# Kernel tuning notes

Hardware: AMD Instinct MI355X
Metric: run time of the kernel (lower is better)

Reference implementation:

```python
import jax, jax.numpy as jnp
import numpy as np

E = 8        # num_local_experts
H = 2048     # hidden_size
I = 4096     # intermediate_size
TOP_K = 1    # num_experts_per_tok
B, S = 2, 1024


def setup_inputs() -> dict:
    key = jax.random.key(0)
    ks = jax.random.split(key, 8)
    sc = 0.02
    return {
        "hidden_states": jax.random.normal(ks[0], (B, S, H), dtype=jnp.float32),
        "router_w": jax.random.normal(ks[1], (E, H), dtype=jnp.float32) * sc,      # torch Linear weight [out,in]
        "gate_up_proj": jax.random.normal(ks[2], (E, H, 2 * I), dtype=jnp.float32) * sc,
        "down_proj": jax.random.normal(ks[3], (E, I, H), dtype=jnp.float32) * sc,
        "shared_gate": jax.random.normal(ks[4], (H, I), dtype=jnp.float32) * sc,
        "shared_up": jax.random.normal(ks[5], (H, I), dtype=jnp.float32) * sc,
        "shared_down": jax.random.normal(ks[6], (I, H), dtype=jnp.float32) * sc,
    }


def reference(hidden_states, router_w, gate_up_proj, down_proj, shared_gate, shared_up, shared_down):
    x = hidden_states.reshape(-1, H)                      # [T, H]
    T = x.shape[0]

    # Router: top-k logits kept, rest -> -inf, then sigmoid (Llama4 sigmoid routing)
    logits = jnp.einsum('th,eh->te', x, router_w)          # [T, E]
    topv, topi = jax.lax.top_k(logits, TOP_K)
    scores = jnp.full_like(logits, -jnp.inf)
    scores = scores.at[jnp.arange(T)[:, None], topi].set(topv)
    router_scores = jax.nn.sigmoid(scores.astype(jnp.float32)).astype(x.dtype).T  # [E, T]

    # Dense dispatch: every token goes to every expert, scaled by its (mostly-zero) score
    routed_in = x[None, :, :] * router_scores[:, :, None]  # [E, T, H]

    # Per-expert gated MLP as one grouped einsum
    gu = jnp.einsum('eth,ehf->etf', routed_in, gate_up_proj)   # [E, T, 2I]
    gate, up = gu[..., :I], gu[..., I:]
    routed_out = jnp.einsum('eti,eih->eth', jax.nn.silu(gate) * up, down_proj)  # [E, T, H]

    # Shared expert on raw tokens
    shared = (jax.nn.silu(x @ shared_gate) * (x @ shared_up)) @ shared_down     # [T, H]

    # scatter_add over full index range == sum over expert axis
    out = shared + routed_out.sum(axis=0)
    return out, router_scores
```

## Files before the change

kernel.cpp:

```cpp
#include <hip/hip_runtime.h>
#include <hip/hip_bf16.h>

#define NE 8
#define TT 2048
#define HD 2048
#define ID 4096

typedef __attribute__((ext_vector_type(8))) short bf16x8;
typedef __attribute__((ext_vector_type(4))) float f32x4;
typedef __attribute__((ext_vector_type(4))) unsigned int u32x4;
typedef __attribute__((ext_vector_type(4))) unsigned short u16x4;
typedef __attribute__((ext_vector_type(8))) unsigned short u16x8;

__device__ __forceinline__ unsigned short f2bf(float f) {
  unsigned int u = __builtin_bit_cast(unsigned int, f);
  u += 0x7FFFu + ((u >> 16) & 1u);
  return (unsigned short)(u >> 16);
}

__global__ void init_kernel(int* counts) {
  if (threadIdx.x < NE) counts[threadIdx.x] = 0;
}

__global__ __launch_bounds__(256) void router_kernel(
    const float* __restrict__ x, const float* __restrict__ rw,
    float* __restrict__ rs_out, unsigned short* __restrict__ xb,
    unsigned short* __restrict__ xsb, int* __restrict__ counts,
    int* __restrict__ tlist) {
  const int t = blockIdx.x;
  const int tid = threadIdx.x;
  const float* xr = x + (size_t)t * HD;
  float acc[NE];
#pragma unroll
  for (int e = 0; e < NE; ++e) acc[e] = 0.f;
  for (int h = tid; h < HD; h += 256) {
    float xv = xr[h];
#pragma unroll
    for (int e = 0; e < NE; ++e) acc[e] += xv * rw[e * HD + h];
  }
#pragma unroll
  for (int e = 0; e < NE; ++e) {
#pragma unroll
    for (int off = 32; off > 0; off >>= 1) acc[e] += __shfl_down(acc[e], off);
  }
  __shared__ float part[4][NE];
  __shared__ int sE;
  __shared__ float sS;
  const int wave = tid >> 6, lane = tid & 63;
  if (lane == 0) {
#pragma unroll
    for (int e = 0; e < NE; ++e) part[wave][e] = acc[e];
  }
  __syncthreads();
  if (tid == 0) {
    float best = -3.4e38f;
    int be = 0;
#pragma unroll
    for (int e = 0; e < NE; ++e) {
      float v = part[0][e] + part[1][e] + part[2][e] + part[3][e];
      if (v > best) { best = v; be = e; }
    }
    float s = 1.f / (1.f + expf(-best));
    sE = be;
    sS = s;
    int pos = atomicAdd(&counts[be], 1);
    tlist[be * TT + pos] = t;
  }
  __syncthreads();
  if (tid < NE) rs_out[tid * TT + t] = (tid == sE) ? sS : 0.f;
  const float s = sS;
  for (int h = tid; h < HD; h += 256) {
    float f = xr[h];
    xb[(size_t)t * HD + h] = f2bf(f);
    xsb[(size_t)t * HD + h] = f2bf(f * s);
  }
}

__global__ __launch_bounds__(256) void tconv_kernel(
    const float* __restrict__ shg, const float* __restrict__ shu,
    const float* __restrict__ shd, unsigned short* __restrict__ shgT,
    unsigned short* __restrict__ shuT, unsigned short* __restrict__ shdT) {
  const int z = blockIdx.z;
  const float* src;
  unsigned short* dst;
  int K, N;
  if (z == 0)      { src = shg; dst = shgT; K = HD; N = ID; }
  else if (z == 1) { src = shu; dst = shuT; K = HD; N = ID; }
  else             { src = shd; dst = shdT; K = ID; N = HD; }
  const int kb = blockIdx.y * 64, nb = blockIdx.x * 64;
  if (kb >= K || nb >= N) return;
  __shared__ unsigned short tile[64][68];
  const int tid = threadIdx.x;
  const int rr = tid >> 4, cc = (tid & 15) * 4;
#pragma unroll
  for (int it = 0; it < 4; ++it) {
    int r = rr + it * 16;
    f32x4 v = *(const f32x4*)(const void*)(src + (size_t)(kb + r) * N + nb + cc);
    tile[r][cc + 0] = f2bf(v[0]);
    tile[r][cc + 1] = f2bf(v[1]);
    tile[r][cc + 2] = f2bf(v[2]);
    tile[r][cc + 3] = f2bf(v[3]);
  }
  __syncthreads();
  const int nr = tid >> 2, kc = (tid & 3) * 16;
#pragma unroll
  for (int h = 0; h < 2; ++h) {
    u16x8 w;
#pragma unroll
    for (int j = 0; j < 8; ++j) w[j] = tile[kc + h * 8 + j][nr];
    *(u16x8*)(void*)(dst + (size_t)(nb + nr) * K + kb + kc + h * 8) = w;
  }
}

__global__ __launch_bounds__(256) void gateup_kernel(
    const unsigned short* __restrict__ xb, const unsigned short* __restrict__ xsb,
    const float* __restrict__ gup, const float* __restrict__ shg,
    const float* __restrict__ shu, const unsigned short* __restrict__ shgT,
    const unsigned short* __restrict__ shuT, const int* __restrict__ counts,
    const int* __restrict__ tlist, unsigned short* __restrict__ hsh,
    unsigned short* __restrict__ hrt, const int shbf) {
  const int bz = blockIdx.z;
  const bool sh = (bz == NE);
  const int cnt = sh ? TT : counts[bz];
  const int row0 = blockIdx.y * 128;
  if (row0 >= cnt) return;
  const int n0 = blockIdx.x * 64;
  const unsigned short* Aptr = sh ? xb : xsb;
  const bool bfb = sh && (shbf != 0);
  const float *B1, *B2;
  size_t ldb;
  const unsigned short *T1 = nullptr, *T2 = nullptr;
  if (sh) {
    B1 = shg + n0; B2 = shu + n0; ldb = ID;
    T1 = shgT + (size_t)n0 * HD; T2 = shuT + (size_t)n0 * HD;
  } else {
    const float* base = gup + (size_t)bz * HD * 2 * ID;
    B1 = base + n0; B2 = base + ID + n0; ldb = 2 * ID;
  }
  unsigned short* hout = sh ? hsh : hrt;

  __shared__ int toks[128];
  __shared__ __align__(16) unsigned short As[2][128][40];
  __shared__ __align__(16) unsigned short Bg[2][64][40];
  __shared__ __align__(16) unsigned short Bu[2][64][40];

  const int tid = threadIdx.x;
  if (tid < 128) {
    int r = row0 + tid;
    toks[tid] = (r < cnt) ? (sh ? r : tlist[bz * TT + r]) : -1;
  }
  __syncthreads();

  const int lane = tid & 63, wave = tid >> 6;
  const int wm = (wave >> 1) * 64, wn = (wave & 1) * 32;
  const int rA0 = tid >> 2, cA = (tid & 3) * 8, rA1 = rA0 + 64;
  const int tok0 = toks[rA0], tok1 = toks[rA1];
  const unsigned short* ap0 = Aptr + ((tok0 >= 0) ? (size_t)tok0 * HD : 0) + cA;
  const unsigned short* ap1 = Aptr + ((tok1 >= 0) ? (size_t)tok1 * HD : 0) + cA;
  const int nB = tid & 63;
  const int kq0 = tid >> 6;
  const int fm = lane & 15, q = lane >> 4;
  const int nrT = tid >> 2, kcT = (tid & 3) * 8;

  const f32x4 zf = {0.f, 0.f, 0.f, 0.f};
  const u32x4 z4 = {0u, 0u, 0u, 0u};
  f32x4 accg[4][2], accu[4][2];
#pragma unroll
  for (int a = 0; a < 4; ++a)
#pragma unroll
    for (int b = 0; b < 2; ++b) { accg[a][b] = zf; accu[a][b] = zf; }

  u32x4 ra0, ra1, tb1, tb2;
  f32x4 rg0, rg1, ru0, ru1;

#define GU_LOAD(K0)                                                            \
  do {                                                                         \
    ra0 = (tok0 >= 0) ? *(const u32x4*)(const void*)(ap0 + (K0)) : z4;         \
    ra1 = (tok1 >= 0) ? *(const u32x4*)(const void*)(ap1 + (K0)) : z4;         \
    if (bfb) {                                                                 \
      tb1 = *(const u32x4*)(const void*)(T1 + (size_t)nrT * HD + (K0) + kcT);  \
      tb2 = *(const u32x4*)(const void*)(T2 + (size_t)nrT * HD + (K0) + kcT);  \
    } else {                                                                   \
      const float* p1 = B1 + (size_t)((K0) + kq0 * 4) * ldb + nB;              \
      const float* p1b = p1 + 16 * ldb;                                        \
      rg0[0] = p1[0]; rg0[1] = p1[ldb]; rg0[2] = p1[2 * ldb]; rg0[3] = p1[3 * ldb]; \
      rg1[0] = p1b[0]; rg1[1] = p1b[ldb]; rg1[2] = p1b[2 * ldb]; rg1[3] = p1b[3 * ldb]; \
      const float* p2 = B2 + (size_t)((K0) + kq0 * 4) * ldb + nB;              \
      const float* p2b = p2 + 16 * ldb;                                        \
      ru0[0] = p2[0]; ru0[1] = p2[ldb]; ru0[2] = p2[2 * ldb]; ru0[3] = p2[3 * ldb]; \
      ru1[0] = p2b[0]; ru1[1] = p2b[ldb]; ru1[2] = p2b[2 * ldb]; ru1[3] = p2b[3 * ldb]; \
    }                                                                          \
  } while (0)

#define GU_WRITE(BUF)                                                          \
  do {                                                                         \
    *(u32x4*)(void*)&As[BUF][rA0][cA] = ra0;                                   \
    *(u32x4*)(void*)&As[BUF][rA1][cA] = ra1;                                   \
    if (bfb) {                                                                 \
      *(u32x4*)(void*)&Bg[BUF][nrT][kcT] = tb1;                                \
      *(u32x4*)(void*)&Bu[BUF][nrT][kcT] = tb2;                                \
    } else {                                                                   \
      u16x4 w;                                                                 \
      w[0] = f2bf(rg0[0]); w[1] = f2bf(rg0[1]); w[2] = f2bf(rg0[2]); w[3] = f2bf(rg0[3]); \
      *(u16x4*)(void*)&Bg[BUF][nB][kq0 * 4] = w;                               \
      w[0] = f2bf(rg1[0]); w[1] = f2bf(rg1[1]); w[2] = f2bf(rg1[2]); w[3] = f2bf(rg1[3]); \
      *(u16x4*)(void*)&Bg[BUF][nB][kq0 * 4 + 16] = w;                          \
      w[0] = f2bf(ru0[0]); w[1] = f2bf(ru0[1]); w[2] = f2bf(ru0[2]); w[3] = f2bf(ru0[3]); \
      *(u16x4*)(void*)&Bu[BUF][nB][kq0 * 4] = w;                               \
      w[0] = f2bf(ru1[0]); w[1] = f2bf(ru1[1]); w[2] = f2bf(ru1[2]); w[3] = f2bf(ru1[3]); \
      *(u16x4*)(void*)&Bu[BUF][nB][kq0 * 4 + 16] = w;                          \
    }                                                                          \
  } while (0)

  GU_LOAD(0);
  GU_WRITE(0);
  GU_LOAD(32);
  asm volatile("s_waitcnt lgkmcnt(0)" ::: "memory");
  __builtin_amdgcn_sched_barrier(0);
  __builtin_amdgcn_s_barrier();

  for (int t = 0; t < HD / 32; ++t) {
    const int cur = t & 1;
    bf16x8 af[4], bgf[2], buf2[2];
#pragma unroll
    for (int mt = 0; mt < 4; ++mt)
      af[mt] = __builtin_bit_cast(bf16x8,
               *(const u32x4*)(const void*)&As[cur][wm + mt * 16 + fm][q * 8]);
#pragma unroll
    for (int nt = 0; nt < 2; ++nt) {
      bgf[nt] = __builtin_bit_cast(bf16x8,
                *(const u32x4*)(const void*)&Bg[cur][wn + nt * 16 + fm][q * 8]);
      buf2[nt] = __builtin_bit_cast(bf16x8,
                 *(const u32x4*)(const void*)&Bu[cur][wn + nt * 16 + fm][q * 8]);
    }
    if (t + 1 < HD / 32) GU_WRITE(cur ^ 1);
    if (t + 2 < HD / 32) GU_LOAD((t + 2) * 32);
    __builtin_amdgcn_s_setprio(1);
#pragma unroll
    for (int mt = 0; mt < 4; ++mt)
#pragma unroll
      for (int nt = 0; nt < 2; ++nt) {
        accg[mt][nt] = __builtin_amdgcn_mfma_f32_16x16x32_bf16(af[mt], bgf[nt], accg[mt][nt], 0, 0, 0);
        accu[mt][nt] = __builtin_amdgcn_mfma_f32_16x16x32_bf16(af[mt], buf2[nt], accu[mt][nt], 0, 0, 0);
      }
    __builtin_amdgcn_s_setprio(0);
    asm volatile("s_waitcnt lgkmcnt(0)" ::: "memory");
    __builtin_amdgcn_sched_barrier(0);
    __builtin_amdgcn_s_barrier();
  }
#undef GU_LOAD
#undef GU_WRITE

#pragma unroll
  for (int mt = 0; mt < 4; ++mt)
#pragma unroll
    for (int nt = 0; nt < 2; ++nt)
#pragma unroll
      for (int r = 0; r < 4; ++r) {
        int ml = wm + mt * 16 + q * 4 + r;
        if (row0 + ml < cnt) {
          int tok = toks[ml];
          int n = n0 + wn + nt * 16 + fm;
          float g = accg[mt][nt][r], u = accu[mt][nt][r];
          float hv = g / (1.f + __expf(-g)) * u;
          hout[(size_t)tok * ID + n] = f2bf(hv);
        }
      }
}

__global__ __launch_bounds__(256) void down_kernel(
    const unsigned short* __restrict__ Ah, const float* __restrict__ Bbase,
    const unsigned short* __restrict__ BT, const int* __restrict__ counts,
    const int* __restrict__ tlist, float* __restrict__ out,
    const int routed, const int shbf) {
  const int e = blockIdx.z;
  const int cnt = routed ? counts[e] : TT;
  const int row0 = blockIdx.y * 128;
  if (row0 >= cnt) return;
  const int n0 = blockIdx.x * 64;
  const bool bfb = (!routed) && (shbf != 0);
  const float* B = routed ? (Bbase + (size_t)e * ID * HD + n0) : (Bbase + n0);
  const unsigned short* T = BT + (size_t)n0 * ID;

  __shared__ int toks[128];
  __shared__ __align__(16) unsigned short As[2][128][40];
  __shared__ __align__(16) unsigned short Bs[2][64][40];

  const int tid = threadIdx.x;
  if (tid < 128) {
    int r = row0 + tid;
    toks[tid] = (r < cnt) ? (routed ? tlist[e * TT + r] : r) : -1;
  }
  __syncthreads();

  const int lane = tid & 63, wave = tid >> 6;
  const int wm = (wave >> 1) * 64, wn = (wave & 1) * 32;
  const int rA0 = tid >> 2, cA = (tid & 3) * 8, rA1 = rA0 + 64;
  const int tok0 = toks[rA0], tok1 = toks[rA1];
  const unsigned short* ap0 = Ah + ((tok0 >= 0) ? (size_t)tok0 * ID : 0) + cA;
  const unsigned short* ap1 = Ah + ((tok1 >= 0) ? (size_t)tok1 * ID : 0) + cA;
  const int nB = tid & 63;
  const int kq0 = tid >> 6;
  const int fm = lane & 15, q = lane >> 4;
  const int nrT = tid >> 2, kcT = (tid & 3) * 8;

  const f32x4 zf = {0.f, 0.f, 0.f, 0.f};
  const u32x4 z4 = {0u, 0u, 0u, 0u};
  f32x4 acc[4][2];
#pragma unroll
  for (int a = 0; a < 4; ++a)
#pragma unroll
    for (int b = 0; b < 2; ++b) acc[a][b] = zf;

  u32x4 ra0, ra1, tb;
  f32x4 rb0, rb1;

#define DN_LOAD(K0)                                                            \
  do {                                                                         \
    ra0 = (tok0 >= 0) ? *(const u32x4*)(const void*)(ap0 + (K0)) : z4;         \
    ra1 = (tok1 >= 0) ? *(const u32x4*)(const void*)(ap1 + (K0)) : z4;         \
    if (bfb) {                                                                 \
      tb = *(const u32x4*)(const void*)(T + (size_t)nrT * ID + (K0) + kcT);    \
    } else {                                                                   \
      const float* p = B + (size_t)((K0) + kq0 * 4) * HD + nB;                 \
      const float* pb = p + 16 * HD;                                           \
      rb0[0] = p[0]; rb0[1] = p[HD]; rb0[2] = p[2 * HD]; rb0[3] = p[3 * HD];   \
      rb1[0] = pb[0]; rb1[1] = pb[HD]; rb1[2] = pb[2 * HD]; rb1[3] = pb[3 * HD]; \
    }                                                                          \
  } while (0)

#define DN_WRITE(BUF)                                                          \
  do {                                                                         \
    *(u32x4*)(void*)&As[BUF][rA0][cA] = ra0;                                   \
    *(u32x4*)(void*)&As[BUF][rA1][cA] = ra1;                                   \
    if (bfb) {                                                                 \
      *(u32x4*)(void*)&Bs[BUF][nrT][kcT] = tb;                                 \
    } else {                                                                   \
      u16x4 w;                                                                 \
      w[0] = f2bf(rb0[0]); w[1] = f2bf(rb0[1]); w[2] = f2bf(rb0[2]); w[3] = f2bf(rb0[3]); \
      *(u16x4*)(void*)&Bs[BUF][nB][kq0 * 4] = w;                               \
      w[0] = f2bf(rb1[0]); w[1] = f2bf(rb1[1]); w[2] = f2bf(rb1[2]); w[3] = f2bf(rb1[3]); \
      *(u16x4*)(void*)&Bs[BUF][nB][kq0 * 4 + 16] = w;                          \
    }                                                                          \
  } while (0)

  DN_LOAD(0);
  DN_WRITE(0);
  DN_LOAD(32);
  asm volatile("s_waitcnt lgkmcnt(0)" ::: "memory");
  __builtin_amdgcn_sched_barrier(0);
  __builtin_amdgcn_s_barrier();

  for (int t = 0; t < ID / 32; ++t) {
    const int cur = t & 1;
    bf16x8 af[4], bfr[2];
#pragma unroll
    for (int mt = 0; mt < 4; ++mt)
      af[mt] = __builtin_bit_cast(bf16x8,
               *(const u32x4*)(const void*)&As[cur][wm + mt * 16 + fm][q * 8]);
#pragma unroll
    for (int nt = 0; nt < 2; ++nt)
      bfr[nt] = __builtin_bit_cast(bf16x8,
                *(const u32x4*)(const void*)&Bs[cur][wn + nt * 16 + fm][q * 8]);
    if (t + 1 < ID / 32) DN_WRITE(cur ^ 1);
    if (t + 2 < ID / 32) DN_LOAD((t + 2) * 32);
    __builtin_amdgcn_s_setprio(1);
#pragma unroll
    for (int mt = 0; mt < 4; ++mt)
#pragma unroll
      for (int nt = 0; nt < 2; ++nt)
        acc[mt][nt] = __builtin_amdgcn_mfma_f32_16x16x32_bf16(af[mt], bfr[nt], acc[mt][nt], 0, 0, 0);
    __builtin_amdgcn_s_setprio(0);
    asm volatile("s_waitcnt lgkmcnt(0)" ::: "memory");
    __builtin_amdgcn_sched_barrier(0);
    __builtin_amdgcn_s_barrier();
  }
#undef DN_LOAD
#undef DN_WRITE

#pragma unroll
  for (int mt = 0; mt < 4; ++mt)
#pragma unroll
    for (int nt = 0; nt < 2; ++nt)
#pragma unroll
      for (int r = 0; r < 4; ++r) {
        int ml = wm + mt * 16 + q * 4 + r;
        if (row0 + ml < cnt) {
          int tok = toks[ml];
          int n = n0 + wn + nt * 16 + fm;
          float v = acc[mt][nt][r];
          float* o = out + (size_t)tok * HD + n;
          if (routed) *o += v; else *o = v;
        }
      }
}

extern "C" void kernel_launch(void* const* d_in, const int* in_sizes, int n_in,
                              void* d_out, int out_size, void* d_ws, size_t ws_size,
                              hipStream_t stream) {
  const float* x   = (const float*)d_in[0];
  const float* rw  = (const float*)d_in[1];
  const float* gup = (const float*)d_in[2];
  const float* dwn = (const float*)d_in[3];
  const float* shg = (const float*)d_in[4];
  const float* shu = (const float*)d_in[5];
  const float* shd = (const float*)d_in[6];
  float* out = (float*)d_out;

  char* ws = (char*)d_ws;
  int* counts = (int*)ws;
  int* tlist = (int*)(ws + 1024);
  unsigned short* xb  = (unsigned short*)(ws + (1 << 17));
  unsigned short* xsb = (unsigned short*)(ws + (1 << 17) + 8388608);
  unsigned short* hsh = (unsigned short*)(ws + (1 << 17) + 16777216);
  unsigned short* hrt = (unsigned short*)(ws + (1 << 17) + 33554432);
  const size_t WB = (size_t)(1 << 17) + 50331648;
  unsigned short* shgT = (unsigned short*)(ws + WB);
  unsigned short* shuT = (unsigned short*)(ws + WB + 16777216);
  unsigned short* shdT = (unsigned short*)(ws + WB + 33554432);
  const size_t need = WB + 3ull * 16777216ull;
  const int shbf = (ws_size >= need) ? 1 : 0;

  hipLaunchKernelGGL(init_kernel, dim3(1), dim3(64), 0, stream, counts);
  hipLaunchKernelGGL(router_kernel, dim3(TT), dim3(256), 0, stream,
                     x, rw, out + (size_t)TT * HD, xb, xsb, counts, tlist);
  if (shbf)
    hipLaunchKernelGGL(tconv_kernel, dim3(64, 64, 3), dim3(256), 0, stream,
                       shg, shu, shd, shgT, shuT, shdT);
  hipLaunchKernelGGL(gateup_kernel, dim3(ID / 64, TT / 128, NE + 1), dim3(256), 0, stream,
                     xb, xsb, gup, shg, shu, shgT, shuT, counts, tlist, hsh, hrt, shbf);
  hipLaunchKernelGGL(down_kernel, dim3(HD / 64, TT / 128, 1), dim3(256), 0, stream,
                     hsh, shd, shdT, counts, tlist, out, 0, shbf);
  hipLaunchKernelGGL(down_kernel, dim3(HD / 64, TT / 128, NE), dim3(256), 0, stream,
                     hrt, dwn, shdT, counts, tlist, out, 1, shbf);
}
```

Baseline: 1.351 ms.

## Split MoE GEMM kernels into specialized routed/shared variants and reorder pipeline

```diff
diff --git a/kernel.cpp b/kernel.cpp
--- a/kernel.cpp
+++ b/kernel.cpp
@@ -9,13 +9,12 @@
 typedef __attribute__((ext_vector_type(8))) short bf16x8;
 typedef __attribute__((ext_vector_type(4))) float f32x4;
 typedef __attribute__((ext_vector_type(4))) unsigned int u32x4;
+typedef __attribute__((ext_vector_type(2))) unsigned int u32x2;
 typedef __attribute__((ext_vector_type(4))) unsigned short u16x4;
 typedef __attribute__((ext_vector_type(8))) unsigned short u16x8;
 
 __device__ __forceinline__ unsigned short f2bf(float f) {
-  unsigned int u = __builtin_bit_cast(unsigned int, f);
-  u += 0x7FFFu + ((u >> 16) & 1u);
-  return (unsigned short)(u >> 16);
+  return __builtin_bit_cast(unsigned short, __float2bfloat16(f));
 }
 
 __global__ void init_kernel(int* counts) {
@@ -112,42 +111,29 @@
   }
 }
 
-__global__ __launch_bounds__(256) void gateup_kernel(
-    const unsigned short* __restrict__ xb, const unsigned short* __restrict__ xsb,
-    const float* __restrict__ gup, const float* __restrict__ shg,
-    const float* __restrict__ shu, const unsigned short* __restrict__ shgT,
-    const unsigned short* __restrict__ shuT, const int* __restrict__ counts,
-    const int* __restrict__ tlist, unsigned short* __restrict__ hsh,
-    unsigned short* __restrict__ hrt, const int shbf) {
-  const int bz = blockIdx.z;
-  const bool sh = (bz == NE);
-  const int cnt = sh ? TT : counts[bz];
+__global__ __launch_bounds__(256) void gu_routed_kernel(
+    const unsigned short* __restrict__ xsb, const float* __restrict__ gup,
+    const int* __restrict__ counts, const int* __restrict__ tlist,
+    unsigned short* __restrict__ hrt) {
+  const int e = blockIdx.z;
+  const int cnt = counts[e];
   const int row0 = blockIdx.y * 128;
   if (row0 >= cnt) return;
   const int n0 = blockIdx.x * 64;
-  const unsigned short* Aptr = sh ? xb : xsb;
-  const bool bfb = sh && (shbf != 0);
-  const float *B1, *B2;
-  size_t ldb;
-  const unsigned short *T1 = nullptr, *T2 = nullptr;
-  if (sh) {
-    B1 = shg + n0; B2 = shu + n0; ldb = ID;
-    T1 = shgT + (size_t)n0 * HD; T2 = shuT + (size_t)n0 * HD;
-  } else {
-    const float* base = gup + (size_t)bz * HD * 2 * ID;
-    B1 = base + n0; B2 = base + ID + n0; ldb = 2 * ID;
-  }
-  unsigned short* hout = sh ? hsh : hrt;
+  const float* Bb = gup + (size_t)e * HD * (2 * ID);
+  const float* B1 = Bb + n0;
+  const float* B2 = Bb + ID + n0;
+  const size_t ldb = 2 * ID;
 
   __shared__ int toks[128];
   __shared__ __align__(16) unsigned short As[2][128][40];
-  __shared__ __align__(16) unsigned short Bg[2][64][40];
-  __shared__ __align__(16) unsigned short Bu[2][64][40];
+  __shared__ __align__(16) unsigned short Bg[2][64][36];
+  __shared__ __align__(16) unsigned short Bu[2][64][36];
 
   const int tid = threadIdx.x;
   if (tid < 128) {
     int r = row0 + tid;
-    toks[tid] = (r < cnt) ? (sh ? r : tlist[bz * TT + r]) : -1;
+    toks[tid] = (r < cnt) ? tlist[e * TT + r] : -1;
   }
   __syncthreads();
 
@@ -155,15 +141,145 @@
   const int wm = (wave >> 1) * 64, wn = (wave & 1) * 32;
   const int rA0 = tid >> 2, cA = (tid & 3) * 8, rA1 = rA0 + 64;
   const int tok0 = toks[rA0], tok1 = toks[rA1];
-  const unsigned short* ap0 = Aptr + ((tok0 >= 0) ? (size_t)tok0 * HD : 0) + cA;
-  const unsigned short* ap1 = Aptr + ((tok1 >= 0) ? (size_t)tok1 * HD : 0) + cA;
+  const unsigned short* ap0 = xsb + ((tok0 >= 0) ? (size_t)tok0 * HD : 0) + cA;
+  const unsigned short* ap1 = xsb + ((tok1 >= 0) ? (size_t)tok1 * HD : 0) + cA;
+  const int nB = tid & 63;
+  const int kq0 = tid >> 6;
+  const int fm = lane & 15, q = lane >> 4;
+
+  const f32x4 zf = {0.f, 0.f, 0.f, 0.f};
+  const u32x4 z4 = {0u, 0u, 0u, 0u};
+  f32x4 accg[4][2], accu[4][2];
+#pragma unroll
+  for (int a = 0; a < 4; ++a)
+#pragma unroll
+    for (int b = 0; b < 2; ++b) { accg[a][b] = zf; accu[a][b] = zf; }
+
+  u32x4 ra0, ra1;
+  f32x4 rg0, rg1, ru0, ru1;
+
+#define LD(K0)                                                                 \
+  do {                                                                         \
+    ra0 = (tok0 >= 0) ? *(const u32x4*)(const void*)(ap0 + (K0)) : z4;         \
+    ra1 = (tok1 >= 0) ? *(const u32x4*)(const void*)(ap1 + (K0)) : z4;         \
+    const float* p1 = B1 + (size_t)((K0) + kq0 * 4) * ldb + nB;                \
+    const float* p1b = p1 + 16 * ldb;                                          \
+    rg0[0] = p1[0]; rg0[1] = p1[ldb]; rg0[2] = p1[2 * ldb]; rg0[3] = p1[3 * ldb]; \
+    rg1[0] = p1b[0]; rg1[1] = p1b[ldb]; rg1[2] = p1b[2 * ldb]; rg1[3] = p1b[3 * ldb]; \
+    const float* p2 = B2 + (size_t)((K0) + kq0 * 4) * ldb + nB;                \
+    const float* p2b = p2 + 16 * ldb;                                          \
+    ru0[0] = p2[0]; ru0[1] = p2[ldb]; ru0[2] = p2[2 * ldb]; ru0[3] = p2[3 * ldb]; \
+    ru1[0] = p2b[0]; ru1[1] = p2b[ldb]; ru1[2] = p2b[2 * ldb]; ru1[3] = p2b[3 * ldb]; \
+  } while (0)
+
+#define WR(BUF)                                                                \
+  do {                                                                         \
+    *(u32x4*)(void*)&As[BUF][rA0][cA] = ra0;                                   \
+    *(u32x4*)(void*)&As[BUF][rA1][cA] = ra1;                                   \
+    u16x4 w;                                                                   \
+    w[0] = f2bf(rg0[0]); w[1] = f2bf(rg0[1]); w[2] = f2bf(rg0[2]); w[3] = f2bf(rg0[3]); \
+    *(u16x4*)(void*)&Bg[BUF][nB][kq0 * 4] = w;                                 \
+    w[0] = f2bf(rg1[0]); w[1] = f2bf(rg1[1]); w[2] = f2bf(rg1[2]); w[3] = f2bf(rg1[3]); \
+    *(u16x4*)(void*)&Bg[BUF][nB][kq0 * 4 + 16] = w;                            \
+    w[0] = f2bf(ru0[0]); w[1] = f2bf(ru0[1]); w[2] = f2bf(ru0[2]); w[3] = f2bf(ru0[3]); \
+    *(u16x4*)(void*)&Bu[BUF][nB][kq0 * 4] = w;                                 \
+    w[0] = f2bf(ru1[0]); w[1] = f2bf(ru1[1]); w[2] = f2bf(ru1[2]); w[3] = f2bf(ru1[3]); \
+    *(u16x4*)(void*)&Bu[BUF][nB][kq0 * 4 + 16] = w;                            \
+  } while (0)
+
+  LD(0);
+  WR(0);
+  LD(32);
+  asm volatile("s_waitcnt lgkmcnt(0)" ::: "memory");
+  __builtin_amdgcn_sched_barrier(0);
+  __builtin_amdgcn_s_barrier();
+
+  constexpr int NT = HD / 32;
+  for (int t = 0; t < NT; ++t) {
+    const int cur = t & 1;
+    bf16x8 af[4], bgf[2], bud[2];
+#pragma unroll
+    for (int mt = 0; mt < 4; ++mt)
+      af[mt] = __builtin_bit_cast(bf16x8,
+               *(const u32x4*)(const void*)&As[cur][wm + mt * 16 + fm][q * 8]);
+#pragma unroll
+    for (int nt = 0; nt < 2; ++nt) {
+      const unsigned short* bp = &Bg[cur][wn + nt * 16 + fm][q * 8];
+      u32x2 lo = *(const u32x2*)(const void*)bp;
+      u32x2 hi = *(const u32x2*)(const void*)(bp + 4);
+      u32x4 v; v[0] = lo[0]; v[1] = lo[1]; v[2] = hi[0]; v[3] = hi[1];
+      bgf[nt] = __builtin_bit_cast(bf16x8, v);
+      const unsigned short* bp2 = &Bu[cur][wn + nt * 16 + fm][q * 8];
+      lo = *(const u32x2*)(const void*)bp2;
+      hi = *(const u32x2*)(const void*)(bp2 + 4);
+      v[0] = lo[0]; v[1] = lo[1]; v[2] = hi[0]; v[3] = hi[1];
+      bud[nt] = __builtin_bit_cast(bf16x8, v);
+    }
+    __builtin_amdgcn_s_setprio(1);
+#pragma unroll
+    for (int mt = 0; mt < 4; ++mt)
+#pragma unroll
+      for (int nt = 0; nt < 2; ++nt) {
+        accg[mt][nt] = __builtin_amdgcn_mfma_f32_16x16x32_bf16(af[mt], bgf[nt], accg[mt][nt], 0, 0, 0);
+        accu[mt][nt] = __builtin_amdgcn_mfma_f32_16x16x32_bf16(af[mt], bud[nt], accu[mt][nt], 0, 0, 0);
+      }
+    __builtin_amdgcn_s_setprio(0);
+    __builtin_amdgcn_sched_barrier(0);
+    if (t + 1 < NT) WR(cur ^ 1);
+    if (t + 2 < NT) LD((t + 2) * 32);
+    asm volatile("s_waitcnt lgkmcnt(0)" ::: "memory");
+    __builtin_amdgcn_sched_barrier(0);
+    __builtin_amdgcn_s_barrier();
+  }
+#undef LD
+#undef WR
+
+#pragma unroll
+  for (int mt = 0; mt < 4; ++mt)
+#pragma unroll
+    for (int nt = 0; nt < 2; ++nt)
+#pragma unroll
+      for (int r = 0; r < 4; ++r) {
+        int ml = wm + mt * 16 + q * 4 + r;
+        if (row0 + ml < cnt) {
+          int tok = toks[ml];
+          int n = n0 + wn + nt * 16 + fm;
+          float g = accg[mt][nt][r], u = accu[mt][nt][r];
+          float hv = g / (1.f + __expf(-g)) * u;
+          hrt[(size_t)tok * ID + n] = f2bf(hv);
+        }
+      }
+}
+
+template <int BF>
+__global__ __launch_bounds__(256) void gu_shared_kernel(
+    const unsigned short* __restrict__ xb, const float* __restrict__ shg,
+    const float* __restrict__ shu, const unsigned short* __restrict__ shgT,
+    const unsigned short* __restrict__ shuT, unsigned short* __restrict__ hsh) {
+  const int row0 = blockIdx.y * 128;
+  const int n0 = blockIdx.x * 64;
+  const float* B1 = shg + n0;
+  const float* B2 = shu + n0;
+  const size_t ldb = ID;
+  const unsigned short* T1 = shgT + (size_t)n0 * HD;
+  const unsigned short* T2 = shuT + (size_t)n0 * HD;
+
+  __shared__ __align__(16) unsigned short As[2][128][40];
+  __shared__ __align__(16) unsigned short Bg[2][64][36];
+  __shared__ __align__(16) unsigned short Bu[2][64][36];
+
+  const int tid = threadIdx.x;
+  const int lane = tid & 63, wave = tid >> 6;
+  const int wm = (wave >> 1) * 64, wn = (wave & 1) * 32;
+  const int rA0 = tid >> 2, cA = (tid & 3) * 8, rA1 = rA0 + 64;
+  const unsigned short* ap0 = xb + (size_t)(row0 + rA0) * HD + cA;
+  const unsigned short* ap1 = xb + (size_t)(row0 + rA1) * HD + cA;
   const int nB = tid & 63;
   const int kq0 = tid >> 6;
   const int fm = lane & 15, q = lane >> 4;
   const int nrT = tid >> 2, kcT = (tid & 3) * 8;
 
   const f32x4 zf = {0.f, 0.f, 0.f, 0.f};
-  const u32x4 z4 = {0u, 0u, 0u, 0u};
   f32x4 accg[4][2], accu[4][2];
 #pragma unroll
   for (int a = 0; a < 4; ++a)
@@ -173,11 +289,11 @@
   u32x4 ra0, ra1, tb1, tb2;
   f32x4 rg0, rg1, ru0, ru1;
 
-#define GU_LOAD(K0)                                                            \
-  do {                                                                         \
-    ra0 = (tok0 >= 0) ? *(const u32x4*)(const void*)(ap0 + (K0)) : z4;         \
-    ra1 = (tok1 >= 0) ? *(const u32x4*)(const void*)(ap1 + (K0)) : z4;         \
-    if (bfb) {                                                                 \
+#define LD(K0)                                                                 \
+  do {                                                                         \
+    ra0 = *(const u32x4*)(const void*)(ap0 + (K0));                            \
+    ra1 = *(const u32x4*)(const void*)(ap1 + (K0));                            \
+    if constexpr (BF) {                                                        \
       tb1 = *(const u32x4*)(const void*)(T1 + (size_t)nrT * HD + (K0) + kcT);  \
       tb2 = *(const u32x4*)(const void*)(T2 + (size_t)nrT * HD + (K0) + kcT);  \
     } else {                                                                   \
@@ -192,13 +308,18 @@
     }                                                                          \
   } while (0)
 
-#define GU_WRITE(BUF)                                                          \
+#define WR(BUF)                                                                \
   do {                                                                         \
     *(u32x4*)(void*)&As[BUF][rA0][cA] = ra0;                                   \
     *(u32x4*)(void*)&As[BUF][rA1][cA] = ra1;                                   \
-    if (bfb) {                                                                 \
-      *(u32x4*)(void*)&Bg[BUF][nrT][kcT] = tb1;                                \
-      *(u32x4*)(void*)&Bu[BUF][nrT][kcT] = tb2;                                \
+    if constexpr (BF) {                                                        \
+      u32x2 lo, hi;                                                            \
+      lo[0] = tb1[0]; lo[1] = tb1[1]; hi[0] = tb1[2]; hi[1] = tb1[3];          \
+      *(u32x2*)(void*)&Bg[BUF][nrT][kcT] = lo;                                 \
+      *(u32x2*)(void*)&Bg[BUF][nrT][kcT + 4] = hi;                             \
+      lo[0] = tb2[0]; lo[1] = tb2[1]; hi[0] = tb2[2]; hi[1] = tb2[3];          \
+      *(u32x2*)(void*)&Bu[BUF][nrT][kcT] = lo;                                 \
+      *(u32x2*)(void*)&Bu[BUF][nrT][kcT + 4] = hi;                             \
     } else {                                                                   \
       u16x4 w;                                                                 \
       w[0] = f2bf(rg0[0]); w[1] = f2bf(rg0[1]); w[2] = f2bf(rg0[2]); w[3] = f2bf(rg0[3]); \
@@ -212,44 +333,52 @@
     }                                                                          \
   } while (0)
 
-  GU_LOAD(0);
-  GU_WRITE(0);
-  GU_LOAD(32);
+  LD(0);
+  WR(0);
+  LD(32);
   asm volatile("s_waitcnt lgkmcnt(0)" ::: "memory");
   __builtin_amdgcn_sched_barrier(0);
   __builtin_amdgcn_s_barrier();
 
-  for (int t = 0; t < HD / 32; ++t) {
+  constexpr int NT = HD / 32;
+  for (int t = 0; t < NT; ++t) {
     const int cur = t & 1;
-    bf16x8 af[4], bgf[2], buf2[2];
+    bf16x8 af[4], bgf[2], bud[2];
 #pragma unroll
     for (int mt = 0; mt < 4; ++mt)
       af[mt] = __builtin_bit_cast(bf16x8,
                *(const u32x4*)(const void*)&As[cur][wm + mt * 16 + fm][q * 8]);
 #pragma unroll
     for (int nt = 0; nt < 2; ++nt) {
-      bgf[nt] = __builtin_bit_cast(bf16x8,
-                *(const u32x4*)(const void*)&Bg[cur][wn + nt * 16 + fm][q * 8]);
-      buf2[nt] = __builtin_bit_cast(bf16x8,
-                 *(const u32x4*)(const void*)&Bu[cur][wn + nt * 16 + fm][q * 8]);
+      const unsigned short* bp = &Bg[cur][wn + nt * 16 + fm][q * 8];
+      u32x2 lo = *(const u32x2*)(const void*)bp;
+      u32x2 hi = *(const u32x2*)(const void*)(bp + 4);
+      u32x4 v; v[0] = lo[0]; v[1] = lo[1]; v[2] = hi[0]; v[3] = hi[1];
+      bgf[nt] = __builtin_bit_cast(bf16x8, v);
+      const unsigned short* bp2 = &Bu[cur][wn + nt * 16 + fm][q * 8];
+      lo = *(const u32x2*)(const void*)bp2;
+      hi = *(const u32x2*)(const void*)(bp2 + 4);
+      v[0] = lo[0]; v[1] = lo[1]; v[2] = hi[0]; v[3] = hi[1];
+      bud[nt] = __builtin_bit_cast(bf16x8, v);
     }
-    if (t + 1 < HD / 32) GU_WRITE(cur ^ 1);
-    if (t + 2 < HD / 32) GU_LOAD((t + 2) * 32);
     __builtin_amdgcn_s_setprio(1);
 #pragma unroll
     for (int mt = 0; mt < 4; ++mt)
 #pragma unroll
       for (int nt = 0; nt < 2; ++nt) {
         accg[mt][nt] = __builtin_amdgcn_mfma_f32_16x16x32_bf16(af[mt], bgf[nt], accg[mt][nt], 0, 0, 0);
-        accu[mt][nt] = __builtin_amdgcn_mfma_f32_16x16x32_bf16(af[mt], buf2[nt], accu[mt][nt], 0, 0, 0);
+        accu[mt][nt] = __builtin_amdgcn_mfma_f32_16x16x32_bf16(af[mt], bud[nt], accu[mt][nt], 0, 0, 0);
       }
     __builtin_amdgcn_s_setprio(0);
+    __builtin_amdgcn_sched_barrier(0);
+    if (t + 1 < NT) WR(cur ^ 1);
+    if (t + 2 < NT) LD((t + 2) * 32);
     asm volatile("s_waitcnt lgkmcnt(0)" ::: "memory");
     __builtin_amdgcn_sched_barrier(0);
     __builtin_amdgcn_s_barrier();
   }
-#undef GU_LOAD
-#undef GU_WRITE
+#undef LD
+#undef WR
 
 #pragma unroll
   for (int mt = 0; mt < 4; ++mt)
@@ -257,55 +386,38 @@
     for (int nt = 0; nt < 2; ++nt)
 #pragma unroll
       for (int r = 0; r < 4; ++r) {
-        int ml = wm + mt * 16 + q * 4 + r;
-        if (row0 + ml < cnt) {
-          int tok = toks[ml];
-          int n = n0 + wn + nt * 16 + fm;
-          float g = accg[mt][nt][r], u = accu[mt][nt][r];
-          float hv = g / (1.f + __expf(-g)) * u;
-          hout[(size_t)tok * ID + n] = f2bf(hv);
-        }
+        int row = row0 + wm + mt * 16 + q * 4 + r;
+        int n = n0 + wn + nt * 16 + fm;
+        float g = accg[mt][nt][r], u = accu[mt][nt][r];
+        float hv = g / (1.f + __expf(-g)) * u;
+        hsh[(size_t)row * ID + n] = f2bf(hv);
       }
 }
 
-__global__ __launch_bounds__(256) void down_kernel(
-    const unsigned short* __restrict__ Ah, const float* __restrict__ Bbase,
-    const unsigned short* __restrict__ BT, const int* __restrict__ counts,
-    const int* __restrict__ tlist, float* __restrict__ out,
-    const int routed, const int shbf) {
-  const int e = blockIdx.z;
-  const int cnt = routed ? counts[e] : TT;
+template <int BF>
+__global__ __launch_bounds__(256) void dn_shared_kernel(
+    const unsigned short* __restrict__ hsh, const float* __restrict__ shd,
+    const unsigned short* __restrict__ shdT, float* __restrict__ out) {
   const int row0 = blockIdx.y * 128;
-  if (row0 >= cnt) return;
   const int n0 = blockIdx.x * 64;
-  const bool bfb = (!routed) && (shbf != 0);
-  const float* B = routed ? (Bbase + (size_t)e * ID * HD + n0) : (Bbase + n0);
-  const unsigned short* T = BT + (size_t)n0 * ID;
-
-  __shared__ int toks[128];
+  const float* B = shd + n0;
+  const unsigned short* T = shdT + (size_t)n0 * ID;
+
   __shared__ __align__(16) unsigned short As[2][128][40];
-  __shared__ __align__(16) unsigned short Bs[2][64][40];
+  __shared__ __align__(16) unsigned short Bs[2][64][36];
 
   const int tid = threadIdx.x;
-  if (tid < 128) {
-    int r = row0 + tid;
-    toks[tid] = (r < cnt) ? (routed ? tlist[e * TT + r] : r) : -1;
-  }
-  __syncthreads();
-
   const int lane = tid & 63, wave = tid >> 6;
   const int wm = (wave >> 1) * 64, wn = (wave & 1) * 32;
   const int rA0 = tid >> 2, cA = (tid & 3) * 8, rA1 = rA0 + 64;
-  const int tok0 = toks[rA0], tok1 = toks[rA1];
-  const unsigned short* ap0 = Ah + ((tok0 >= 0) ? (size_t)tok0 * ID : 0) + cA;
-  const unsigned short* ap1 = Ah + ((tok1 >= 0) ? (size_t)tok1 * ID : 0) + cA;
+  const unsigned short* ap0 = hsh + (size_t)(row0 + rA0) * ID + cA;
+  const unsigned short* ap1 = hsh + (size_t)(row0 + rA1) * ID + cA;
   const int nB = tid & 63;
   const int kq0 = tid >> 6;
   const int fm = lane & 15, q = lane >> 4;
   const int nrT = tid >> 2, kcT = (tid & 3) * 8;
 
   const f32x4 zf = {0.f, 0.f, 0.f, 0.f};
-  const u32x4 z4 = {0u, 0u, 0u, 0u};
   f32x4 acc[4][2];
 #pragma unroll
   for (int a = 0; a < 4; ++a)
@@ -315,11 +427,11 @@
   u32x4 ra0, ra1, tb;
   f32x4 rb0, rb1;
 
-#define DN_LOAD(K0)                                                            \
-  do {                                                                         \
-    ra0 = (tok0 >= 0) ? *(const u32x4*)(const void*)(ap0 + (K0)) : z4;         \
-    ra1 = (tok1 >= 0) ? *(const u32x4*)(const void*)(ap1 + (K0)) : z4;         \
-    if (bfb) {                                                                 \
+#define LD(K0)                                                                 \
+  do {                                                                         \
+    ra0 = *(const u32x4*)(const void*)(ap0 + (K0));                            \
+    ra1 = *(const u32x4*)(const void*)(ap1 + (K0));                            \
+    if constexpr (BF) {                                                        \
       tb = *(const u32x4*)(const void*)(T + (size_t)nrT * ID + (K0) + kcT);    \
     } else {                                                                   \
       const float* p = B + (size_t)((K0) + kq0 * 4) * HD + nB;                 \
@@ -329,12 +441,15 @@
     }                                                                          \
   } while (0)
 
-#define DN_WRITE(BUF)                                                          \
+#define WR(BUF)                                                                \
   do {                                                                         \
     *(u32x4*)(void*)&As[BUF][rA0][cA] = ra0;                                   \
     *(u32x4*)(void*)&As[BUF][rA1][cA] = ra1;                                   \
-    if (bfb) {                                                                 \
-      *(u32x4*)(void*)&Bs[BUF][nrT][kcT] = tb;                                 \
+    if constexpr (BF) {                                                        \
+      u32x2 lo, hi;                                                            \
+      lo[0] = tb[0]; lo[1] = tb[1]; hi[0] = tb[2]; hi[1] = tb[3];              \
+      *(u32x2*)(void*)&Bs[BUF][nrT][kcT] = lo;                                 \
+      *(u32x2*)(void*)&Bs[BUF][nrT][kcT + 4] = hi;                             \
     } else {                                                                   \
       u16x4 w;                                                                 \
       w[0] = f2bf(rb0[0]); w[1] = f2bf(rb0[1]); w[2] = f2bf(rb0[2]); w[3] = f2bf(rb0[3]); \
@@ -344,14 +459,15 @@
     }                                                                          \
   } while (0)
 
-  DN_LOAD(0);
-  DN_WRITE(0);
-  DN_LOAD(32);
+  LD(0);
+  WR(0);
+  LD(32);
   asm volatile("s_waitcnt lgkmcnt(0)" ::: "memory");
   __builtin_amdgcn_sched_barrier(0);
   __builtin_amdgcn_s_barrier();
 
-  for (int t = 0; t < ID / 32; ++t) {
+  constexpr int NT = ID / 32;
+  for (int t = 0; t < NT; ++t) {
     const int cur = t & 1;
     bf16x8 af[4], bfr[2];
 #pragma unroll
@@ -359,11 +475,13 @@
       af[mt] = __builtin_bit_cast(bf16x8,
                *(const u32x4*)(const void*)&As[cur][wm + mt * 16 + fm][q * 8]);
 #pragma unroll
-    for (int nt = 0; nt < 2; ++nt)
-      bfr[nt] = __builtin_bit_cast(bf16x8,
-                *(const u32x4*)(const void*)&Bs[cur][wn + nt * 16 + fm][q * 8]);
-    if (t + 1 < ID / 32) DN_WRITE(cur ^ 1);
-    if (t + 2 < ID / 32) DN_LOAD((t + 2) * 32);
+    for (int nt = 0; nt < 2; ++nt) {
+      const unsigned short* bp = &Bs[cur][wn + nt * 16 + fm][q * 8];
+      u32x2 lo = *(const u32x2*)(const void*)bp;
+      u32x2 hi = *(const u32x2*)(const void*)(bp + 4);
+      u32x4 v; v[0] = lo[0]; v[1] = lo[1]; v[2] = hi[0]; v[3] = hi[1];
+      bfr[nt] = __builtin_bit_cast(bf16x8, v);
+    }
     __builtin_amdgcn_s_setprio(1);
 #pragma unroll
     for (int mt = 0; mt < 4; ++mt)
@@ -371,12 +489,131 @@
       for (int nt = 0; nt < 2; ++nt)
         acc[mt][nt] = __builtin_amdgcn_mfma_f32_16x16x32_bf16(af[mt], bfr[nt], acc[mt][nt], 0, 0, 0);
     __builtin_amdgcn_s_setprio(0);
+    __builtin_amdgcn_sched_barrier(0);
+    if (t + 1 < NT) WR(cur ^ 1);
+    if (t + 2 < NT) LD((t + 2) * 32);
     asm volatile("s_waitcnt lgkmcnt(0)" ::: "memory");
     __builtin_amdgcn_sched_barrier(0);
     __builtin_amdgcn_s_barrier();
   }
-#undef DN_LOAD
-#undef DN_WRITE
+#undef LD
+#undef WR
+
+#pragma unroll
+  for (int mt = 0; mt < 4; ++mt)
+#pragma unroll
+    for (int nt = 0; nt < 2; ++nt)
+#pragma unroll
+      for (int r = 0; r < 4; ++r) {
+        int row = row0 + wm + mt * 16 + q * 4 + r;
+        int n = n0 + wn + nt * 16 + fm;
+        out[(size_t)row * HD + n] = acc[mt][nt][r];
+      }
+}
+
+__global__ __launch_bounds__(256) void dn_routed_kernel(
+    const unsigned short* __restrict__ hrt, const float* __restrict__ dwn,
+    const int* __restrict__ counts, const int* __restrict__ tlist,
+    float* __restrict__ out) {
+  const int e = blockIdx.z;
+  const int cnt = counts[e];
+  const int row0 = blockIdx.y * 128;
+  if (row0 >= cnt) return;
+  const int n0 = blockIdx.x * 64;
+  const float* B = dwn + (size_t)e * ID * HD + n0;
+
+  __shared__ int toks[128];
+  __shared__ __align__(16) unsigned short As[2][128][40];
+  __shared__ __align__(16) unsigned short Bs[2][64][36];
+
+  const int tid = threadIdx.x;
+  if (tid < 128) {
+    int r = row0 + tid;
+    toks[tid] = (r < cnt) ? tlist[e * TT + r] : -1;
+  }
+  __syncthreads();
+
+  const int lane = tid & 63, wave = tid >> 6;
+  const int wm = (wave >> 1) * 64, wn = (wave & 1) * 32;
+  const int rA0 = tid >> 2, cA = (tid & 3) * 8, rA1 = rA0 + 64;
+  const int tok0 = toks[rA0], tok1 = toks[rA1];
+  const unsigned short* ap0 = hrt + ((tok0 >= 0) ? (size_t)tok0 * ID : 0) + cA;
+  const unsigned short* ap1 = hrt + ((tok1 >= 0) ? (size_t)tok1 * ID : 0) + cA;
+  const int nB = tid & 63;
+  const int kq0 = tid >> 6;
+  const int fm = lane & 15, q = lane >> 4;
+
+  const f32x4 zf = {0.f, 0.f, 0.f, 0.f};
+  const u32x4 z4 = {0u, 0u, 0u, 0u};
+  f32x4 acc[4][2];
+#pragma unroll
+  for (int a = 0; a < 4; ++a)
+#pragma unroll
+    for (int b = 0; b < 2; ++b) acc[a][b] = zf;
+
+  u32x4 ra0, ra1;
+  f32x4 rb0, rb1;
+
+#define LD(K0)                                                                 \
+  do {                                                                         \
+    ra0 = (tok0 >= 0) ? *(const u32x4*)(const void*)(ap0 + (K0)) : z4;         \
+    ra1 = (tok1 >= 0) ? *(const u32x4*)(const void*)(ap1 + (K0)) : z4;         \
+    const float* p = B + (size_t)((K0) + kq0 * 4) * HD + nB;                   \
+    const float* pb = p + 16 * HD;                                             \
+    rb0[0] = p[0]; rb0[1] = p[HD]; rb0[2] = p[2 * HD]; rb0[3] = p[3 * HD];     \
+    rb1[0] = pb[0]; rb1[1] = pb[HD]; rb1[2] = pb[2 * HD]; rb1[3] = pb[3 * HD]; \
+  } while (0)
+
+#define WR(BUF)                                                                \
+  do {                                                                         \
+    *(u32x4*)(void*)&As[BUF][rA0][cA] = ra0;                                   \
+    *(u32x4*)(void*)&As[BUF][rA1][cA] = ra1;                                   \
+    u16x4 w;                                                                   \
+    w[0] = f2bf(rb0[0]); w[1] = f2bf(rb0[1]); w[2] = f2bf(rb0[2]); w[3] = f2bf(rb0[3]); \
+    *(u16x4*)(void*)&Bs[BUF][nB][kq0 * 4] = w;                                 \
+    w[0] = f2bf(rb1[0]); w[1] = f2bf(rb1[1]); w[2] = f2bf(rb1[2]); w[3] = f2bf(rb1[3]); \
+    *(u16x4*)(void*)&Bs[BUF][nB][kq0 * 4 + 16] = w;                            \
+  } while (0)
+
+  LD(0);
+  WR(0);
+  LD(32);
+  asm volatile("s_waitcnt lgkmcnt(0)" ::: "memory");
+  __builtin_amdgcn_sched_barrier(0);
+  __builtin_amdgcn_s_barrier();
+
+  constexpr int NT = ID / 32;
+  for (int t = 0; t < NT; ++t) {
+    const int cur = t & 1;
+    bf16x8 af[4], bfr[2];
+#pragma unroll
+    for (int mt = 0; mt < 4; ++mt)
+      af[mt] = __builtin_bit_cast(bf16x8,
+               *(const u32x4*)(const void*)&As[cur][wm + mt * 16 + fm][q * 8]);
+#pragma unroll
+    for (int nt = 0; nt < 2; ++nt) {
+      const unsigned short* bp = &Bs[cur][wn + nt * 16 + fm][q * 8];
+      u32x2 lo = *(const u32x2*)(const void*)bp;
+      u32x2 hi = *(const u32x2*)(const void*)(bp + 4);
+      u32x4 v; v[0] = lo[0]; v[1] = lo[1]; v[2] = hi[0]; v[3] = hi[1];
+      bfr[nt] = __builtin_bit_cast(bf16x8, v);
+    }
+    __builtin_amdgcn_s_setprio(1);
+#pragma unroll
+    for (int mt = 0; mt < 4; ++mt)
+#pragma unroll
+      for (int nt = 0; nt < 2; ++nt)
+        acc[mt][nt] = __builtin_amdgcn_mfma_f32_16x16x32_bf16(af[mt], bfr[nt], acc[mt][nt], 0, 0, 0);
+    __builtin_amdgcn_s_setprio(0);
+    __builtin_amdgcn_sched_barrier(0);
+    if (t + 1 < NT) WR(cur ^ 1);
+    if (t + 2 < NT) LD((t + 2) * 32);
+    asm volatile("s_waitcnt lgkmcnt(0)" ::: "memory");
+    __builtin_amdgcn_sched_barrier(0);
+    __builtin_amdgcn_s_barrier();
+  }
+#undef LD
+#undef WR
 
 #pragma unroll
   for (int mt = 0; mt < 4; ++mt)
@@ -388,9 +625,7 @@
         if (row0 + ml < cnt) {
           int tok = toks[ml];
           int n = n0 + wn + nt * 16 + fm;
-          float v = acc[mt][nt][r];
-          float* o = out + (size_t)tok * HD + n;
-          if (routed) *o += v; else *o = v;
+          out[(size_t)tok * HD + n] += acc[mt][nt][r];
         }
       }
 }
@@ -427,10 +662,20 @@
   if (shbf)
     hipLaunchKernelGGL(tconv_kernel, dim3(64, 64, 3), dim3(256), 0, stream,
                        shg, shu, shd, shgT, shuT, shdT);
-  hipLaunchKernelGGL(gateup_kernel, dim3(ID / 64, TT / 128, NE + 1), dim3(256), 0, stream,
-                     xb, xsb, gup, shg, shu, shgT, shuT, counts, tlist, hsh, hrt, shbf);
-  hipLaunchKernelGGL(down_kernel, dim3(HD / 64, TT / 128, 1), dim3(256), 0, stream,
-                     hsh, shd, shdT, counts, tlist, out, 0, shbf);
-  hipLaunchKernelGGL(down_kernel, dim3(HD / 64, TT / 128, NE), dim3(256), 0, stream,
-                     hrt, dwn, shdT, counts, tlist, out, 1, shbf);
-}
+  hipLaunchKernelGGL(gu_routed_kernel, dim3(ID / 64, TT / 128, NE), dim3(256), 0, stream,
+                     xsb, gup, counts, tlist, hrt);
+  if (shbf)
+    hipLaunchKernelGGL((gu_shared_kernel<1>), dim3(ID / 64, TT / 128), dim3(256), 0, stream,
+                       xb, shg, shu, shgT, shuT, hsh);
+  else
+    hipLaunchKernelGGL((gu_shared_kernel<0>), dim3(ID / 64, TT / 128), dim3(256), 0, stream,
+                       xb, shg, shu, shgT, shuT, hsh);
+  if (shbf)
+    hipLaunchKernelGGL((dn_shared_kernel<1>), dim3(HD / 64, TT / 128), dim3(256), 0, stream,
+                       hsh, shd, shdT, out);
+  else
+    hipLaunchKernelGGL((dn_shared_kernel<0>), dim3(HD / 64, TT / 128), dim3(256), 0, stream,
+                       hsh, shd, shdT, out);
+  hipLaunchKernelGGL(dn_routed_kernel, dim3(HD / 64, TT / 128, NE), dim3(256), 0, stream,
+                     hrt, dwn, counts, tlist, out);
+}
```

After: 1.313 ms. 1.03x faster.
